# Optimization experiments

Hardware: AMD Instinct MI355X
Metric: run time of the kernel (lower is better)

Reference implementation:

```python
import jax, jax.numpy as jnp
import numpy as np

B, D, K = 32768, 256, 2048
BETA = 0.25


def setup_inputs() -> dict:
    key = jax.random.key(0)
    k1, k2 = jax.random.split(key)
    latents = jax.random.normal(k1, (B, D), dtype=jnp.float32)
    # nn.Embedding weight initialized uniform(-1/K, 1/K)
    embedding = jax.random.uniform(k2, (K, D), dtype=jnp.float32,
                                   minval=-1.0 / K, maxval=1.0 / K)
    return {"latents": latents, "embedding": embedding}


def reference(latents, embedding):
    # Squared-L2 distances: [B, K]
    dist = (jnp.sum(latents ** 2, axis=1, keepdims=True)
            + jnp.sum(embedding ** 2, axis=1)
            - 2.0 * jnp.matmul(latents, embedding.T))
    encoding_inds = jnp.argmin(dist, axis=1)  # [B]

    # Gather codebook rows (equivalent to one-hot @ embedding)
    quantized = embedding[encoding_inds]  # [B, D]

    commitment_loss = jnp.mean((jax.lax.stop_gradient(quantized) - latents) ** 2)
    embedding_loss = jnp.mean((quantized - jax.lax.stop_gradient(latents)) ** 2)
    vq_loss = commitment_loss * BETA + embedding_loss

    # Straight-through estimator
    quantized_st = latents + jax.lax.stop_gradient(quantized - latents)

    # avg_probs = mean of one-hot over batch == normalized histogram of inds
    counts = jnp.zeros((K,), dtype=jnp.float32).at[encoding_inds].add(1.0)
    avg_probs = counts / B
    entropy_vq = -jnp.sum(avg_probs * jnp.log(avg_probs + 1e-10))

    # dist values at selected codes
    cluster_metric = jnp.mean(
        jnp.take_along_axis(dist, encoding_inds[:, None], axis=1))

    return (quantized_st, vq_loss, entropy_vq,
            encoding_inds[:, None], cluster_metric)
```

## Files before the change

kernel.cpp:

```cpp
#include <hip/hip_runtime.h>
#include <math.h>

#define B_ROWS 32768
#define D_DIM  256
#define K_CODES 2048

#define OUT_Q   0
#define OUT_VQ  8388608
#define OUT_ENT 8388609
#define OUT_IND 8388610
#define OUT_CM  8421378


#define WS_SE2   0
#define WS_SX2   8192
#define WS_CNT   139264
#define WS_PACK  147456
#define WS_MSEP  409600
#define WS_DISTP 475136
#define WS_BCAT  540672

typedef _Float16 f16x8 __attribute__((ext_vector_type(8)));
typedef float f32x4 __attribute__((ext_vector_type(4)));
typedef union { _Float16 h[4]; uint2 u2; } h4pack;

__global__ __launch_bounds__(256) void k_init(
    const float* __restrict__ X, const float* __restrict__ E,
    _Float16* __restrict__ A, _Float16* __restrict__ Bc,
    float* __restrict__ sx2, float* __restrict__ se2,
    unsigned long long* __restrict__ packed, int* __restrict__ counts) {
  int w = threadIdx.x >> 6, lane = threadIdx.x & 63;
  if (blockIdx.x < 8192) {
    int row = blockIdx.x * 4 + w;
    float4 v = ((const float4*)(X + (size_t)row * D_DIM))[lane];
    float s = v.x * v.x + v.y * v.y + v.z * v.z + v.w * v.w;
#pragma unroll
    for (int off = 32; off > 0; off >>= 1) s += __shfl_xor(s, off, 64);
    if (lane == 0) { sx2[row] = s; packed[row] = ~0ull; }
    h4pack hi, lo;
    hi.h[0] = (_Float16)v.x; hi.h[1] = (_Float16)v.y;
    hi.h[2] = (_Float16)v.z; hi.h[3] = (_Float16)v.w;
    lo.h[0] = (_Float16)((v.x - (float)hi.h[0]) * 4096.0f);
    lo.h[1] = (_Float16)((v.y - (float)hi.h[1]) * 4096.0f);
    lo.h[2] = (_Float16)((v.z - (float)hi.h[2]) * 4096.0f);
    lo.h[3] = (_Float16)((v.w - (float)hi.h[3]) * 4096.0f);
    *(uint2*)&A[(size_t)row * 512 + 4 * lane] = hi.u2;
    *(uint2*)&A[(size_t)row * 512 + 256 + 4 * lane] = lo.u2;
  } else {
    int bb = blockIdx.x - 8192;
    int row = bb * 4 + w;
    if (threadIdx.x < 4) counts[bb * 4 + threadIdx.x] = 0;
    float4 v = ((const float4*)(E + (size_t)row * D_DIM))[lane];
    float s = v.x * v.x + v.y * v.y + v.z * v.z + v.w * v.w;
#pragma unroll
    for (int off = 32; off > 0; off >>= 1) s += __shfl_xor(s, off, 64);
    if (lane == 0) se2[row] = s;
    const float S = 4194304.0f;
    const float SH = 0.000244140625f;
    float e0 = v.x * S, e1 = v.y * S, e2 = v.z * S, e3 = v.w * S;
    h4pack b1, b2, b3;
    b1.h[0] = (_Float16)e0; b1.h[1] = (_Float16)e1;
    b1.h[2] = (_Float16)e2; b1.h[3] = (_Float16)e3;
    b2.h[0] = (_Float16)((float)b1.h[0] * SH);
    b2.h[1] = (_Float16)((float)b1.h[1] * SH);
    b2.h[2] = (_Float16)((float)b1.h[2] * SH);
    b2.h[3] = (_Float16)((float)b1.h[3] * SH);
    b3.h[0] = (_Float16)(e0 - (float)b1.h[0]);
    b3.h[1] = (_Float16)(e1 - (float)b1.h[1]);
    b3.h[2] = (_Float16)(e2 - (float)b1.h[2]);
    b3.h[3] = (_Float16)(e3 - (float)b1.h[3]);
    *(uint2*)&Bc[(size_t)row * 768 + 4 * lane] = b1.u2;
    *(uint2*)&Bc[(size_t)row * 768 + 256 + 4 * lane] = b2.u2;
    *(uint2*)&Bc[(size_t)row * 768 + 512 + 4 * lane] = b3.u2;
  }
}

__global__ __launch_bounds__(256, 4) void k_mfma(
    const _Float16* __restrict__ A, const _Float16* __restrict__ Bc,
    const float* __restrict__ se2, const float* __restrict__ sx2,
    unsigned long long* __restrict__ packed) {
  __shared__ _Float16 As[2][128 * 32];
  __shared__ _Float16 Bs[2][128 * 32];
  const int tid = threadIdx.x;
  const int w = tid >> 6, lane = tid & 63;
  const int rowblk = blockIdx.x & 255, cg = blockIdx.x >> 8;
  const int row0 = rowblk * 128, col00 = cg * 256;
  const int lr = lane >> 2, lc = lane & 3;
  const int q = lane >> 4, c = lane & 15;
  const int wr = (w >> 1) * 64, wc = (w & 1) * 64;

  float4 srow[4];
#pragma unroll
  for (int i = 0; i < 4; ++i)
    srow[i] = *(const float4*)&sx2[row0 + wr + i * 16 + q * 4];

  const char* Abase = (const char*)A;
  const char* Bbase = (const char*)Bc;

  auto issue = [&](int ct_i, int ktl_i, int bsel) {
    int a_off = (ktl_i < 8) ? ktl_i * 64
              : (ktl_i < 16) ? 512 + (ktl_i - 8) * 64 : (ktl_i - 16) * 64;
    int b_off = ktl_i * 64;
    int colb = col00 + ct_i * 128;
#pragma unroll
    for (int t = 0; t < 2; ++t) {
      int s = w * 2 + t;
      const char* ga =
          Abase + (((size_t)(row0 + s * 16 + lr)) << 10) + a_off + lc * 16;
      const char* gb =
          Bbase + ((size_t)(colb + s * 16 + lr)) * 1536 + b_off + lc * 16;
      __builtin_amdgcn_global_load_lds(
          (const __attribute__((address_space(1))) unsigned int*)ga,
          (__attribute__((address_space(3))) unsigned int*)((char*)&As[bsel][0] +
                                                            s * 1024),
          16, 0, 0);
      __builtin_amdgcn_global_load_lds(
          (const __attribute__((address_space(1))) unsigned int*)gb,
          (__attribute__((address_space(3))) unsigned int*)((char*)&Bs[bsel][0] +
                                                            s * 1024),
          16, 0, 0);
    }
  };

  issue(0, 0, 0);

  const float inv = 4.76837158203125e-07f;
  for (int ct = 0; ct < 2; ++ct) {
    f32x4 acc[4][4];
#pragma unroll
    for (int i = 0; i < 4; i++)
#pragma unroll
      for (int j = 0; j < 4; j++) acc[i][j] = (f32x4){0.f, 0.f, 0.f, 0.f};

#pragma unroll 2
    for (int ktl = 0; ktl < 24; ++ktl) {
      __syncthreads();
      int gidx = ct * 24 + ktl + 1;
      if (gidx < 48) issue(gidx / 24, gidx % 24, (ktl + 1) & 1);
      const int b = ktl & 1;
      f16x8 af[4], bf[4];
#pragma unroll
      for (int i = 0; i < 4; ++i) {
        af[i] = *(const f16x8*)&As[b][(wr + i * 16 + c) * 32 + q * 8];
        bf[i] = *(const f16x8*)&Bs[b][(wc + i * 16 + c) * 32 + q * 8];
      }
#pragma unroll
      for (int i = 0; i < 4; ++i)
#pragma unroll
        for (int j = 0; j < 4; ++j)
          acc[i][j] = __builtin_amdgcn_mfma_f32_16x16x32_f16(af[i], bf[j],
                                                             acc[i][j], 0, 0, 0);
    }

    int colb = col00 + ct * 128;
    float se_j[4];
#pragma unroll
    for (int j = 0; j < 4; ++j) se_j[j] = se2[colb + wc + j * 16 + c];
#pragma unroll
    for (int i = 0; i < 4; ++i) {
#pragma unroll
      for (int r = 0; r < 4; ++r) {
        int lrow = wr + i * 16 + q * 4 + r;
        float sx = ((const float*)&srow[i])[r];
        float bs = 3.402823466e38f;
        int bk = 0;
#pragma unroll
        for (int j = 0; j < 4; ++j) {
          float t1 = sx + se_j[j];
          float d = t1 - acc[i][j][r] * inv;
          if (d < bs) { bs = d; bk = colb + wc + j * 16 + c; }
        }
#pragma unroll
        for (int off = 1; off < 16; off <<= 1) {
          float os = __shfl_xor(bs, off, 64);
          int ok = __shfl_xor(bk, off, 64);
          if (os < bs || (os == bs && ok < bk)) { bs = os; bk = ok; }
        }
        if (c == 0) {
          unsigned long long v =
              ((unsigned long long)__float_as_uint(bs) << 32) |
              (unsigned long long)(unsigned int)bk;
          atomicMin(&packed[row0 + lrow], v);
        }
      }
    }
  }
}

__global__ __launch_bounds__(256) void k_gather(
    const float* __restrict__ X, const float* __restrict__ E,
    const unsigned long long* __restrict__ packed, float* __restrict__ outq,
    float* __restrict__ out_ind, int* __restrict__ counts,
    double* __restrict__ msep, double* __restrict__ distp) {
  __shared__ int sk[16];
  __shared__ float sd[16];
  int tid = threadIdx.x;
  if (tid < 16) {
    int row = blockIdx.x * 16 + tid;
    unsigned long long v = packed[row];
    int k = (int)(v & 0xFFFFFFFFull);
    sk[tid] = k;
    sd[tid] = __uint_as_float((unsigned int)(v >> 32));
    out_ind[row] = (float)k;
    atomicAdd(&counts[k], 1);
  }
  __syncthreads();
  int wave = tid >> 6, lane = tid & 63;
  double msum = 0.0, dsum = 0.0;
#pragma unroll
  for (int rr = 0; rr < 4; rr++) {
    int li = wave * 4 + rr;
    int b = blockIdx.x * 16 + li;
    int ind = sk[li];
    float4 x4 = ((const float4*)(X + (size_t)b * D_DIM))[lane];
    float4 q4 = ((const float4*)(E + (size_t)ind * D_DIM))[lane];
    float d0 = q4.x - x4.x, d1 = q4.y - x4.y, d2 = q4.z - x4.z, d3 = q4.w - x4.w;
    float4 o;
    o.x = x4.x + d0; o.y = x4.y + d1; o.z = x4.z + d2; o.w = x4.w + d3;
    ((float4*)(outq + (size_t)b * D_DIM))[lane] = o;
    float v = d0 * d0 + d1 * d1 + d2 * d2 + d3 * d3;
#pragma unroll
    for (int off = 32; off > 0; off >>= 1) v += __shfl_xor(v, off, 64);
    if (lane == 0) { msum += (double)v; dsum += (double)sd[li]; }
  }
  if (lane == 0) {
    int wg = blockIdx.x * 4 + wave;
    msep[wg] = msum;
    distp[wg] = dsum;
  }
}

__global__ __launch_bounds__(256) void k_final(
    const int* __restrict__ counts, const double* __restrict__ msep,
    const double* __restrict__ distp, float* __restrict__ out) {
  __shared__ double red[256];
  int t = threadIdx.x;

  double m = 0.0;
  for (int i = t; i < 8192; i += 256) m += msep[i];
  red[t] = m;
  __syncthreads();
  for (int s = 128; s > 0; s >>= 1) {
    if (t < s) red[t] += red[t + s];
    __syncthreads();
  }
  if (t == 0) {
    double mse = red[0] / ((double)B_ROWS * (double)D_DIM);
    out[OUT_VQ] = (float)(mse * 1.25);
  }
  __syncthreads();

  double d = 0.0;
  for (int i = t; i < 8192; i += 256) d += distp[i];
  red[t] = d;
  __syncthreads();
  for (int s = 128; s > 0; s >>= 1) {
    if (t < s) red[t] += red[t + s];
    __syncthreads();
  }
  if (t == 0) out[OUT_CM] = (float)(red[0] / (double)B_ROWS);
  __syncthreads();

  double e = 0.0;
  for (int k = t; k < K_CODES; k += 256) {
    float p = (float)counts[k] * (1.0f / 32768.0f);
    e += (double)(p * logf(p + 1e-10f));
  }
  red[t] = e;
  __syncthreads();
  for (int s = 128; s > 0; s >>= 1) {
    if (t < s) red[t] += red[t + s];
    __syncthreads();
  }
  if (t == 0) out[OUT_ENT] = (float)(-red[0]);
}

extern "C" void kernel_launch(void* const* d_in, const int* in_sizes, int n_in,
                              void* d_out, int out_size, void* d_ws,
                              size_t ws_size, hipStream_t stream) {
  const float* X = (const float*)d_in[0];
  const float* E = (const float*)d_in[1];
  float* out = (float*)d_out;
  char* ws = (char*)d_ws;
  float* se2 = (float*)(ws + WS_SE2);
  float* sx2 = (float*)(ws + WS_SX2);
  int* counts = (int*)(ws + WS_CNT);
  unsigned long long* packed = (unsigned long long*)(ws + WS_PACK);
  double* msep = (double*)(ws + WS_MSEP);
  double* distp = (double*)(ws + WS_DISTP);
  _Float16* Bcat = (_Float16*)(ws + WS_BCAT);
  _Float16* Acat = (_Float16*)d_out;

  k_init<<<8704, 256, 0, stream>>>(X, E, Acat, Bcat, sx2, se2, packed, counts);
  k_mfma<<<2048, 256, 0, stream>>>(Acat, Bcat, se2, sx2, packed);
  k_gather<<<B_ROWS / 16, 256, 0, stream>>>(X, E, packed, out + OUT_Q,
                                            out + OUT_IND, counts, msep, distp);
  k_final<<<1, 256, 0, stream>>>(counts, msep, distp, out);
}
```

Baseline: 275.4 us.

## Rewrite distance GEMM with 256x256 tiles, swizzled LDS and interleaved prefetch

```diff
diff --git a/kernel.cpp b/kernel.cpp
--- a/kernel.cpp
+++ b/kernel.cpp
@@ -75,115 +75,168 @@
   }
 }
 
-__global__ __launch_bounds__(256, 4) void k_mfma(
+#define BARX() asm volatile("s_barrier" ::: "memory")
+
+#define MFMA_QUAD(I0, J0)                                                    \
+  do {                                                                       \
+    __builtin_amdgcn_s_setprio(1);                                           \
+    _Pragma("unroll") for (int ii = 0; ii < 4; ++ii) {                       \
+      _Pragma("unroll") for (int jj = 0; jj < 2; ++jj) {                     \
+        _Pragma("unroll") for (int kk = 0; kk < 2; ++kk) {                   \
+          acc[(I0) + ii][(J0) + jj] =                                        \
+              __builtin_amdgcn_mfma_f32_16x16x32_f16(                        \
+                  af[ii * 2 + kk], bf[jj * 2 + kk],                          \
+                  acc[(I0) + ii][(J0) + jj], 0, 0, 0);                       \
+        }                                                                    \
+      }                                                                      \
+    }                                                                        \
+    __builtin_amdgcn_s_setprio(0);                                           \
+  } while (0)
+
+__global__ __launch_bounds__(512, 2) void k_mfma2(
     const _Float16* __restrict__ A, const _Float16* __restrict__ Bc,
     const float* __restrict__ se2, const float* __restrict__ sx2,
     unsigned long long* __restrict__ packed) {
-  __shared__ _Float16 As[2][128 * 32];
-  __shared__ _Float16 Bs[2][128 * 32];
+  extern __shared__ char smem[];
   const int tid = threadIdx.x;
   const int w = tid >> 6, lane = tid & 63;
-  const int rowblk = blockIdx.x & 255, cg = blockIdx.x >> 8;
-  const int row0 = rowblk * 128, col00 = cg * 256;
-  const int lr = lane >> 2, lc = lane & 3;
+  const int wm = w >> 2, wn = w & 3;
   const int q = lane >> 4, c = lane & 15;
-  const int wr = (w >> 1) * 64, wc = (w & 1) * 64;
-
-  float4 srow[4];
-#pragma unroll
-  for (int i = 0; i < 4; ++i)
-    srow[i] = *(const float4*)&sx2[row0 + wr + i * 16 + q * 4];
+  const int rowb = blockIdx.x & 127, colb = blockIdx.x >> 7;
+  const int rowpan = rowb * 256, colpan = colb * 256;
+  const int rsel = lane >> 3;
+  const int chunkb = ((lane & 7) ^ rsel) * 16;
+  const int rswz = c & 7;
 
   const char* Abase = (const char*)A;
   const char* Bbase = (const char*)Bc;
-
-  auto issue = [&](int ct_i, int ktl_i, int bsel) {
-    int a_off = (ktl_i < 8) ? ktl_i * 64
-              : (ktl_i < 16) ? 512 + (ktl_i - 8) * 64 : (ktl_i - 16) * 64;
-    int b_off = ktl_i * 64;
-    int colb = col00 + ct_i * 128;
-#pragma unroll
-    for (int t = 0; t < 2; ++t) {
-      int s = w * 2 + t;
-      const char* ga =
-          Abase + (((size_t)(row0 + s * 16 + lr)) << 10) + a_off + lc * 16;
-      const char* gb =
-          Bbase + ((size_t)(colb + s * 16 + lr)) * 1536 + b_off + lc * 16;
-      __builtin_amdgcn_global_load_lds(
-          (const __attribute__((address_space(1))) unsigned int*)ga,
-          (__attribute__((address_space(3))) unsigned int*)((char*)&As[bsel][0] +
-                                                            s * 1024),
-          16, 0, 0);
-      __builtin_amdgcn_global_load_lds(
-          (const __attribute__((address_space(1))) unsigned int*)gb,
-          (__attribute__((address_space(3))) unsigned int*)((char*)&Bs[bsel][0] +
-                                                            s * 1024),
-          16, 0, 0);
+  char* sA = smem;
+  char* sB = smem + 65536;
+
+  auto issue = [&](int tt, int g, int bsel) {
+    const int hh = (g == 3 || g == 4 || g == 5 || g == 7) ? 1 : 0;
+    const int ss = (g == 2 || g == 4 || g == 6 || g == 7) ? 1 : 0;
+    const int rl = hh * 128 + ss * 64 + w * 8 + rsel;
+    const char* src;
+    char* dst;
+    if (g == 0 || g >= 5) {
+      int aoff = (tt & 3) * 128 + (((tt >> 2) == 1) ? 512 : 0);
+      src = Abase + ((size_t)(rowpan + rl) << 10) + aoff + chunkb;
+      dst = sA + bsel * 32768 + hh * 16384 + ss * 8192 + w * 1024;
+    } else {
+      src = Bbase + (size_t)(colpan + rl) * 1536 + tt * 128 + chunkb;
+      dst = sB + bsel * 32768 + hh * 16384 + ss * 8192 + w * 1024;
     }
+    __builtin_amdgcn_global_load_lds(
+        (const __attribute__((address_space(1))) unsigned int*)src,
+        (__attribute__((address_space(3))) unsigned int*)dst, 16, 0, 0);
   };
 
-  issue(0, 0, 0);
+  f32x4 acc[8][4];
+#pragma unroll
+  for (int i = 0; i < 8; ++i)
+#pragma unroll
+    for (int j = 0; j < 4; ++j) acc[i][j] = (f32x4){0.f, 0.f, 0.f, 0.f};
+
+  auto lda = [&](f16x8* af, int ihalf, int bsel) {
+#pragma unroll
+    for (int ii = 0; ii < 4; ++ii)
+#pragma unroll
+      for (int kk = 0; kk < 2; ++kk) {
+        int row = wm * 128 + (ihalf * 4 + ii) * 16 + c;
+        int sl = ((kk * 4 + q) ^ rswz) * 16;
+        af[ii * 2 + kk] = *(const f16x8*)(sA + bsel * 32768 + row * 128 + sl);
+      }
+  };
+  auto ldb = [&](f16x8* bf, int j0, int bsel) {
+#pragma unroll
+    for (int jj = 0; jj < 2; ++jj)
+#pragma unroll
+      for (int kk = 0; kk < 2; ++kk) {
+        int col = wn * 64 + (j0 + jj) * 16 + c;
+        int sl = ((kk * 4 + q) ^ rswz) * 16;
+        bf[jj * 2 + kk] = *(const f16x8*)(sB + bsel * 32768 + col * 128 + sl);
+      }
+  };
+
+#pragma unroll
+  for (int g = 0; g < 8; ++g) issue(0, g, 0);
+  asm volatile("s_waitcnt vmcnt(2)" ::: "memory");
+  BARX();
+
+  f16x8 af[8], bf[4];
+
+  for (int t = 0; t < 12; ++t) {
+    const int bsel = t & 1;
+    const int nb = bsel ^ 1;
+    const bool pre = (t < 11);
+    lda(af, 0, bsel);
+    ldb(bf, 0, bsel);
+    if (pre) { issue(t + 1, 0, nb); issue(t + 1, 1, nb); }
+    BARX();
+    MFMA_QUAD(0, 0);
+    BARX();
+    ldb(bf, 2, bsel);
+    if (pre) { issue(t + 1, 2, nb); issue(t + 1, 3, nb); }
+    BARX();
+    MFMA_QUAD(0, 2);
+    if (pre) asm volatile("s_waitcnt vmcnt(4)" ::: "memory");
+    else     asm volatile("s_waitcnt vmcnt(0)" ::: "memory");
+    BARX();
+    lda(af, 1, bsel);
+    if (pre) { issue(t + 1, 4, nb); issue(t + 1, 5, nb); }
+    BARX();
+    MFMA_QUAD(4, 2);
+    BARX();
+    ldb(bf, 0, bsel);
+    if (pre) { issue(t + 1, 6, nb); issue(t + 1, 7, nb); }
+    BARX();
+    MFMA_QUAD(4, 0);
+    if (pre) asm volatile("s_waitcnt vmcnt(2)" ::: "memory");
+    BARX();
+  }
 
   const float inv = 4.76837158203125e-07f;
-  for (int ct = 0; ct < 2; ++ct) {
-    f32x4 acc[4][4];
-#pragma unroll
-    for (int i = 0; i < 4; i++)
-#pragma unroll
-      for (int j = 0; j < 4; j++) acc[i][j] = (f32x4){0.f, 0.f, 0.f, 0.f};
-
-#pragma unroll 2
-    for (int ktl = 0; ktl < 24; ++ktl) {
-      __syncthreads();
-      int gidx = ct * 24 + ktl + 1;
-      if (gidx < 48) issue(gidx / 24, gidx % 24, (ktl + 1) & 1);
-      const int b = ktl & 1;
-      f16x8 af[4], bf[4];
-#pragma unroll
-      for (int i = 0; i < 4; ++i) {
-        af[i] = *(const f16x8*)&As[b][(wr + i * 16 + c) * 32 + q * 8];
-        bf[i] = *(const f16x8*)&Bs[b][(wc + i * 16 + c) * 32 + q * 8];
-      }
-#pragma unroll
-      for (int i = 0; i < 4; ++i)
-#pragma unroll
-        for (int j = 0; j < 4; ++j)
-          acc[i][j] = __builtin_amdgcn_mfma_f32_16x16x32_f16(af[i], bf[j],
-                                                             acc[i][j], 0, 0, 0);
+  float se_j[4];
+#pragma unroll
+  for (int j = 0; j < 4; ++j) se_j[j] = se2[colpan + wn * 64 + j * 16 + c];
+  unsigned long long* m = (unsigned long long*)smem;
+#pragma unroll
+  for (int i = 0; i < 8; ++i) {
+    float4 sx4 = *(const float4*)&sx2[rowpan + wm * 128 + i * 16 + q * 4];
+#pragma unroll
+    for (int r = 0; r < 4; ++r) {
+      float sx = ((const float*)&sx4)[r];
+      float bs = 3.402823466e38f;
+      int bk = 0;
+#pragma unroll
+      for (int j = 0; j < 4; ++j) {
+        float t1 = sx + se_j[j];
+        float d = t1 - acc[i][j][r] * inv;
+        if (d < bs) { bs = d; bk = colpan + wn * 64 + j * 16 + c; }
+      }
+#pragma unroll
+      for (int off = 1; off < 16; off <<= 1) {
+        float os = __shfl_xor(bs, off, 64);
+        int ok = __shfl_xor(bk, off, 64);
+        if (os < bs || (os == bs && ok < bk)) { bs = os; bk = ok; }
+      }
+      if (c == 0) {
+        m[wn * 256 + wm * 128 + i * 16 + q * 4 + r] =
+            ((unsigned long long)__float_as_uint(bs) << 32) |
+            (unsigned long long)(unsigned int)bk;
+      }
     }
-
-    int colb = col00 + ct * 128;
-    float se_j[4];
-#pragma unroll
-    for (int j = 0; j < 4; ++j) se_j[j] = se2[colb + wc + j * 16 + c];
-#pragma unroll
-    for (int i = 0; i < 4; ++i) {
-#pragma unroll
-      for (int r = 0; r < 4; ++r) {
-        int lrow = wr + i * 16 + q * 4 + r;
-        float sx = ((const float*)&srow[i])[r];
-        float bs = 3.402823466e38f;
-        int bk = 0;
-#pragma unroll
-        for (int j = 0; j < 4; ++j) {
-          float t1 = sx + se_j[j];
-          float d = t1 - acc[i][j][r] * inv;
-          if (d < bs) { bs = d; bk = colb + wc + j * 16 + c; }
-        }
-#pragma unroll
-        for (int off = 1; off < 16; off <<= 1) {
-          float os = __shfl_xor(bs, off, 64);
-          int ok = __shfl_xor(bk, off, 64);
-          if (os < bs || (os == bs && ok < bk)) { bs = os; bk = ok; }
-        }
-        if (c == 0) {
-          unsigned long long v =
-              ((unsigned long long)__float_as_uint(bs) << 32) |
-              (unsigned long long)(unsigned int)bk;
-          atomicMin(&packed[row0 + lrow], v);
-        }
-      }
+  }
+  __syncthreads();
+  if (tid < 256) {
+    unsigned long long v = m[tid];
+#pragma unroll
+    for (int mm = 1; mm < 4; ++mm) {
+      unsigned long long o = m[mm * 256 + tid];
+      if (o < v) v = o;
     }
+    atomicMin(&packed[rowpan + tid], v);
   }
 }
 
@@ -291,8 +344,15 @@
   _Float16* Bcat = (_Float16*)(ws + WS_BCAT);
   _Float16* Acat = (_Float16*)d_out;
 
+  static bool attr_done = false;
+  if (!attr_done) {
+    hipFuncSetAttribute((const void*)k_mfma2,
+                        hipFuncAttributeMaxDynamicSharedMemorySize, 131072);
+    attr_done = true;
+  }
+
   k_init<<<8704, 256, 0, stream>>>(X, E, Acat, Bcat, sx2, se2, packed, counts);
-  k_mfma<<<2048, 256, 0, stream>>>(Acat, Bcat, se2, sx2, packed);
+  k_mfma2<<<1024, 512, 131072, stream>>>(Acat, Bcat, se2, sx2, packed);
   k_gather<<<B_ROWS / 16, 256, 0, stream>>>(X, E, packed, out + OUT_Q,
                                             out + OUT_IND, counts, msep, distp);
   k_final<<<1, 256, 0, stream>>>(counts, msep, distp, out);
```

Result: faster. 262.5 us (-4.7%).
